# Optimization experiments

Hardware: AMD Instinct MI355X
Metric: run time of the kernel (lower is better)

## Reference

```python
import jax, jax.numpy as jnp
import numpy as np

B, F, N, D, P = 32, 32, 36, 2048, 512  # batch, frames, objects, input dim, projected dim


def setup_inputs() -> dict:
    key = jax.random.key(0)
    ks = jax.random.split(key, 8)
    s = 1.0 / np.sqrt(D).astype(np.float32)  # torch nn.Linear default init range
    u = lambda k, shape: jax.random.uniform(k, shape, jnp.float32, -s, s)
    return {
        "object_variable": jax.random.normal(ks[0], (B, F, N, D), jnp.float32),
        "W_proj": u(ks[1], (D, P)), "b_proj": u(ks[2], (P,)),
        "W_sigma": u(ks[3], (D, P)), "b_sigma": u(ks[4], (P,)),
        "W_psi": u(ks[5], (D, P)), "b_psi": u(ks[6], (P,)),
        "W_r": u(ks[7], (D, P)),  # bias=False
    }


def reference(object_variable, W_proj, b_proj, W_sigma, b_sigma, W_psi, b_psi, W_r):
    # Dropouts are identity in eval mode.
    x = object_variable                                   # [B,F,N,D]
    r_feat = x @ W_proj + b_proj                          # [B,F,N,P]
    sig = x @ W_sigma + b_sigma                           # [B,F,N,P]
    psi = x @ W_psi + b_psi                               # [B,F,N,P]
    a_coeff = jnp.einsum('bfnp,bfmp->bfnm', sig, psi)     # [B,F,N,N] unscaled QK^T
    a_hat = jax.nn.softmax(a_coeff, axis=-1)
    r_hat = jnp.einsum('bfnm,bfmp->bfnp', a_hat, x @ W_r) # AV matmul
    return (r_feat, r_hat)
```

## Files before the change

kernel.cpp:

```cpp
#include <hip/hip_runtime.h>
#include <hip/hip_fp16.h>
#include <stdint.h>

typedef _Float16 half2v __attribute__((ext_vector_type(2)));
typedef _Float16 half4v __attribute__((ext_vector_type(4)));
typedef _Float16 half8v __attribute__((ext_vector_type(8)));
typedef float    float4v __attribute__((ext_vector_type(4)));

#define KDIM 2048
#define PDIM 512
#define MROWS 36864
#define NOBJ 36
#define NTOT 2048

__device__ __forceinline__ void gload_lds16(const void* g, void* l) {
    using gptr_t = const __attribute__((address_space(1))) unsigned int*;
    using lptr_t = __attribute__((address_space(3))) unsigned int*;
    __builtin_amdgcn_global_load_lds((gptr_t)(uintptr_t)g,
                                     (lptr_t)(uint32_t)(uintptr_t)l,
                                     16, 0, 0);
}

__global__ __launch_bounds__(256)
void cvt_x_kernel(const float* __restrict__ x, _Float16* __restrict__ xh) {
    const size_t i = ((size_t)blockIdx.x * 256 + threadIdx.x) * 8;
    float4v a = *(const float4v*)&x[i];
    float4v b = *(const float4v*)&x[i + 4];
    half8v h;
    h[0] = (_Float16)a[0]; h[1] = (_Float16)a[1];
    h[2] = (_Float16)a[2]; h[3] = (_Float16)a[3];
    h[4] = (_Float16)b[0]; h[5] = (_Float16)b[1];
    h[6] = (_Float16)b[2]; h[7] = (_Float16)b[3];
    *(half8v*)&xh[i] = h;
}

__global__ __launch_bounds__(256)
void cvt_w_kernel(const float* __restrict__ Wp, const float* __restrict__ Ws,
                  const float* __restrict__ Wq, const float* __restrict__ Wr,
                  _Float16* __restrict__ wt) {
    const int bid = blockIdx.x;
    const int mat = bid >> 10;
    const int t   = bid & 1023;
    const int kt  = t >> 4;
    const int pt  = t & 15;
    const float* W = (mat == 0) ? Wp : (mat == 1) ? Ws : (mat == 2) ? Wq : Wr;

    __shared__ float tile[32][33];
    const int tx = threadIdx.x & 31;
    const int ty = threadIdx.x >> 5;
    #pragma unroll
    for (int r = 0; r < 4; ++r) {
        const int k = kt * 32 + ty + r * 8;
        tile[ty + r * 8][tx] = W[(size_t)k * PDIM + pt * 32 + tx];
    }
    __syncthreads();
    #pragma unroll
    for (int r = 0; r < 4; ++r) {
        const int p = pt * 32 + ty + r * 8;
        const int n = mat * PDIM + p;
        wt[(size_t)n * KDIM + kt * 32 + tx] = (_Float16)tile[tx][ty + r * 8];
    }
}

__global__ __launch_bounds__(256, 2)
void proj_gemm(const _Float16* __restrict__ A, const _Float16* __restrict__ Bt,
               float* __restrict__ rfeat, _Float16* __restrict__ sg,
               _Float16* __restrict__ ph, _Float16* __restrict__ vh,
               const float* __restrict__ bp, const float* __restrict__ bs,
               const float* __restrict__ bq) {
    __shared__ _Float16 sA[128 * 32];
    __shared__ _Float16 sB[128 * 32];

    const int tid  = threadIdx.x;
    const int lane = tid & 63;
    const int wave = tid >> 6;

    const int n0 = (blockIdx.x & 15) * 128;
    const int m0 = (blockIdx.x >> 4) * 128;

    const int srow = tid >> 2;
    const int skc  = (tid & 3) * 8;
    const _Float16* ga0 = A  + (size_t)(m0 + srow) * KDIM + skc;
    const _Float16* ga1 = A  + (size_t)(m0 + 64 + srow) * KDIM + skc;
    const _Float16* gb0 = Bt + (size_t)(n0 + srow) * KDIM + skc;
    const _Float16* gb1 = Bt + (size_t)(n0 + 64 + srow) * KDIM + skc;

    char* lA = (char*)sA + tid * 16;
    char* lB = (char*)sB + tid * 16;

    const int m_off = (wave >> 1) * 64;
    const int n_off = (wave & 1) * 64;
    const int frow  = lane & 15;
    const int fk    = (lane >> 4) * 8;

    float4v acc[4][4] = {};

    for (int kt = 0; kt < KDIM / 32; ++kt) {
        __syncthreads();
        gload_lds16(ga0, lA);
        gload_lds16(ga1, lA + 4096);
        gload_lds16(gb0, lB);
        gload_lds16(gb1, lB + 4096);
        ga0 += 32; ga1 += 32; gb0 += 32; gb1 += 32;
        __syncthreads();

        half8v af[4], bf[4];
        #pragma unroll
        for (int i = 0; i < 4; ++i)
            af[i] = *(const half8v*)&sA[(m_off + i * 16 + frow) * 32 + fk];
        #pragma unroll
        for (int j = 0; j < 4; ++j)
            bf[j] = *(const half8v*)&sB[(n_off + j * 16 + frow) * 32 + fk];
        #pragma unroll
        for (int i = 0; i < 4; ++i)
            #pragma unroll
            for (int j = 0; j < 4; ++j)
                acc[i][j] = __builtin_amdgcn_mfma_f32_16x16x32_f16(af[i], bf[j], acc[i][j], 0, 0, 0);
    }

    const int seg = n0 >> 9;
    const int pn0 = (n0 & 511) + n_off;
    #pragma unroll
    for (int j = 0; j < 4; ++j) {
        const int pcol = pn0 + j * 16 + frow;
        float bias = 0.0f;
        if (seg == 0)      bias = bp[pcol];
        else if (seg == 1) bias = bs[pcol];
        else if (seg == 2) bias = bq[pcol];
        #pragma unroll
        for (int i = 0; i < 4; ++i) {
            const int rb = m0 + m_off + i * 16 + (lane >> 4) * 4;
            #pragma unroll
            for (int r = 0; r < 4; ++r) {
                const float val = acc[i][j][r] + bias;
                const size_t off = (size_t)(rb + r) * PDIM + pcol;
                if (seg == 0)      rfeat[off] = val;
                else if (seg == 1) sg[off] = (_Float16)val;
                else if (seg == 2) ph[off] = (_Float16)val;
                else               vh[off] = (_Float16)val;
            }
        }
    }
}

__global__ __launch_bounds__(256, 2)
void attn_kernel(const _Float16* __restrict__ sg, const _Float16* __restrict__ ph,
                 const _Float16* __restrict__ vh, float* __restrict__ rhat) {
    __shared__ _Float16 ss[NOBJ * 520];
    __shared__ _Float16 ps[NOBJ * 520];
    __shared__ float    Ls[NOBJ * 37];

    const int tid = threadIdx.x;
    const size_t base = (size_t)blockIdx.x * (NOBJ * PDIM);

    for (int c = tid; c < (NOBJ * PDIM / 8); c += 256) {
        const int row = c >> 6;
        const int col = (c & 63) * 8;
        *(half8v*)&ss[row * 520 + col] = *(const half8v*)&sg[base + row * PDIM + col];
        *(half8v*)&ps[row * 520 + col] = *(const half8v*)&ph[base + row * PDIM + col];
    }
    __syncthreads();

    if (tid < 144) {
        const int i0 = (tid / 12) * 3;
        const int j0 = (tid % 12) * 3;
        float accv[3][3] = {};
        for (int p = 0; p < PDIM; p += 8) {
            half8v si[3], pj[3];
            #pragma unroll
            for (int ii = 0; ii < 3; ++ii) si[ii] = *(const half8v*)&ss[(i0 + ii) * 520 + p];
            #pragma unroll
            for (int jj = 0; jj < 3; ++jj) pj[jj] = *(const half8v*)&ps[(j0 + jj) * 520 + p];
            #pragma unroll
            for (int ii = 0; ii < 3; ++ii)
                #pragma unroll
                for (int jj = 0; jj < 3; ++jj) {
                    float t = accv[ii][jj];
                    #pragma unroll
                    for (int q = 0; q < 4; ++q) {
                        half2v x2; x2[0] = si[ii][2 * q]; x2[1] = si[ii][2 * q + 1];
                        half2v y2; y2[0] = pj[jj][2 * q]; y2[1] = pj[jj][2 * q + 1];
                        t = __builtin_amdgcn_fdot2(x2, y2, t, false);
                    }
                    accv[ii][jj] = t;
                }
        }
        #pragma unroll
        for (int ii = 0; ii < 3; ++ii)
            #pragma unroll
            for (int jj = 0; jj < 3; ++jj)
                Ls[(i0 + ii) * 37 + (j0 + jj)] = accv[ii][jj];
    }
    __syncthreads();

    if (tid < NOBJ) {
        float mx = -1e30f;
        for (int j = 0; j < NOBJ; ++j) mx = fmaxf(mx, Ls[tid * 37 + j]);
        float sum = 0.0f;
        for (int j = 0; j < NOBJ; ++j) {
            float e = __expf(Ls[tid * 37 + j] - mx);
            sum += e;
            Ls[tid * 37 + j] = e;
        }
        const float inv = 1.0f / sum;
        for (int j = 0; j < NOBJ; ++j) Ls[tid * 37 + j] *= inv;
    }
    __syncthreads();

    const int p4 = (tid & 127) * 4;
    const int r0 = tid >> 7;
    float4v acc[18] = {};
    for (int j = 0; j < NOBJ; ++j) {
        half4v v4 = *(const half4v*)&vh[base + (size_t)j * PDIM + p4];
        float4v vf;
        vf[0] = (float)v4[0]; vf[1] = (float)v4[1];
        vf[2] = (float)v4[2]; vf[3] = (float)v4[3];
        #pragma unroll
        for (int m = 0; m < 18; ++m) {
            const float aw = Ls[(2 * m + r0) * 37 + j];
            acc[m] += aw * vf;
        }
    }
    #pragma unroll
    for (int m = 0; m < 18; ++m)
        *(float4v*)&rhat[base + (size_t)(2 * m + r0) * PDIM + p4] = acc[m];
}

extern "C" void kernel_launch(void* const* d_in, const int* in_sizes, int n_in,
                              void* d_out, int out_size, void* d_ws, size_t ws_size,
                              hipStream_t stream) {
    const float* x   = (const float*)d_in[0];
    const float* Wp  = (const float*)d_in[1];
    const float* bp  = (const float*)d_in[2];
    const float* Wsg = (const float*)d_in[3];
    const float* bsg = (const float*)d_in[4];
    const float* Wps = (const float*)d_in[5];
    const float* bps = (const float*)d_in[6];
    const float* Wr  = (const float*)d_in[7];
    float* out = (float*)d_out;

    char* ws = (char*)d_ws;
    _Float16* xh = (_Float16*)(ws);
    _Float16* wt = (_Float16*)(ws + 150994944UL);
    _Float16* sg = (_Float16*)(ws + 159383552UL);
    _Float16* ph = (_Float16*)(ws + 197132288UL);
    _Float16* vh = (_Float16*)(ws + 234881024UL);

    cvt_x_kernel<<<36864, 256, 0, stream>>>(x, xh);
    cvt_w_kernel<<<4096, 256, 0, stream>>>(Wp, Wsg, Wps, Wr, wt);
    proj_gemm<<<288 * 16, 256, 0, stream>>>(xh, wt, out, sg, ph, vh, bp, bsg, bps);
    attn_kernel<<<1024, 256, 0, stream>>>(sg, ph, vh, out + 18874368);
}
```

Baseline: 905.6 us.

## Rewrite projection GEMM with 256x256 tiles, double-buffered LDS and phased MFMA pipeline

The projection GEMM moves from 128x128 tiles with 256 threads and a single LDS buffer to 256x256 tiles with 512 threads, a K step of 64, and double-buffered LDS. Global-to-LDS loads for the next tiles are issued during MFMA phases, with explicit waitcnt, barriers and setprio. The change also adds XOR swizzling of LDS columns to avoid bank conflicts and a block-index swizzle for L2 locality. The aim is to hide memory latency and raise MFMA utilisation, at the cost of more LDS per block (128KB), higher register pressure, and fragile hand-written synchronisation.

```diff
diff --git a/kernel.cpp b/kernel.cpp
--- a/kernel.cpp
+++ b/kernel.cpp
@@ -12,6 +12,7 @@
 #define MROWS 36864
 #define NOBJ 36
 #define NTOT 2048
+#define KT   32
 
 __device__ __forceinline__ void gload_lds16(const void* g, void* l) {
     using gptr_t = const __attribute__((address_space(1))) unsigned int*;
@@ -62,77 +63,150 @@
     }
 }
 
-__global__ __launch_bounds__(256, 2)
+#define BARRIER() __builtin_amdgcn_s_barrier()
+
+#define STAGE_AH(b_, kt_, h_) do {                                            \
+    const _Float16* g_ = pA + (size_t)(kt_) * 64 + (size_t)(h_) * 262144;     \
+    char* l_ = (char*)sA + (b_) * 32768 + (h_) * 16384 + tid * 16;            \
+    gload_lds16(g_, l_);                                                      \
+    gload_lds16(g_ + 131072, l_ + 8192);                                      \
+} while (0)
+
+#define STAGE_BH(b_, kt_, h_) do {                                            \
+    const _Float16* g_ = pB + (size_t)(kt_) * 64 + (size_t)(h_) * 262144;     \
+    char* l_ = (char*)sB + (b_) * 32768 + (h_) * 16384 + tid * 16;            \
+    gload_lds16(g_, l_);                                                      \
+    gload_lds16(g_ + 131072, l_ + 8192);                                      \
+} while (0)
+
+#define LOAD_AF(b_, qm_) do {                                                 \
+    const char* ba_ = (const char*)sA + (b_) * 32768 + wrbase;                \
+    _Pragma("unroll")                                                         \
+    for (int mi = 0; mi < 4; ++mi) {                                          \
+        const int ro_ = ((qm_) * 64 + mi * 16 + r15) * 128;                   \
+        af[mi][0] = *(const half8v*)(ba_ + ro_ + ck0);                        \
+        af[mi][1] = *(const half8v*)(ba_ + ro_ + ck1);                        \
+    }                                                                         \
+} while (0)
+
+#define LOAD_BF(b_, qn_, dst_) do {                                           \
+    const char* bb_ = (const char*)sB + (b_) * 32768 + wcbase;                \
+    _Pragma("unroll")                                                         \
+    for (int ni = 0; ni < 2; ++ni) {                                          \
+        const int ro_ = (rB0 + (qn_) * 32 + ni * 16 + r15) * 128;             \
+        dst_[ni][0] = *(const half8v*)(bb_ + ro_ + ck0);                      \
+        dst_[ni][1] = *(const half8v*)(bb_ + ro_ + ck1);                      \
+    }                                                                         \
+} while (0)
+
+#define MFMA16(mb_, nb_, bf_) do {                                            \
+    _Pragma("unroll")                                                         \
+    for (int mi = 0; mi < 4; ++mi)                                            \
+        _Pragma("unroll")                                                     \
+        for (int ni = 0; ni < 2; ++ni) {                                      \
+            acc[(mb_) + mi][(nb_) + ni] = __builtin_amdgcn_mfma_f32_16x16x32_f16( \
+                af[mi][0], bf_[ni][0], acc[(mb_) + mi][(nb_) + ni], 0, 0, 0); \
+            acc[(mb_) + mi][(nb_) + ni] = __builtin_amdgcn_mfma_f32_16x16x32_f16( \
+                af[mi][1], bf_[ni][1], acc[(mb_) + mi][(nb_) + ni], 0, 0, 0); \
+        }                                                                     \
+} while (0)
+
+#define PHASE_SYNC() do {                                                     \
+    BARRIER();                                                                \
+    asm volatile("s_waitcnt lgkmcnt(0)" ::: "memory");                        \
+    __builtin_amdgcn_sched_barrier(0);                                        \
+} while (0)
+
+#define ITER(t_, b_) do {                                                     \
+                                                        \
+    LOAD_AF(b_, 0); LOAD_BF(b_, 0, b0);                                       \
+    if ((t_) + 1 < KT) STAGE_AH((b_) ^ 1, (t_) + 1, 0);                       \
+    PHASE_SYNC();                                                             \
+    __builtin_amdgcn_s_setprio(1); MFMA16(0, 0, b0);                          \
+    __builtin_amdgcn_s_setprio(0); BARRIER();                                 \
+                                                        \
+    LOAD_BF(b_, 1, b1);                                                       \
+    if ((t_) + 1 < KT) STAGE_AH((b_) ^ 1, (t_) + 1, 1);                       \
+    PHASE_SYNC();                                                             \
+    __builtin_amdgcn_s_setprio(1); MFMA16(0, 2, b1);                          \
+    __builtin_amdgcn_s_setprio(0); BARRIER();                                 \
+                                                        \
+    LOAD_AF(b_, 1);                                                           \
+    if ((t_) + 2 < KT) STAGE_BH(b_, (t_) + 2, 0);                             \
+    PHASE_SYNC();                                                             \
+    __builtin_amdgcn_s_setprio(1); MFMA16(4, 2, b1);                          \
+    __builtin_amdgcn_s_setprio(0); BARRIER();                                 \
+                      \
+    if ((t_) + 2 < KT) STAGE_BH(b_, (t_) + 2, 1);                             \
+    __builtin_amdgcn_s_setprio(1); MFMA16(4, 0, b0);                          \
+    __builtin_amdgcn_s_setprio(0);                                            \
+    if ((t_) + 2 < KT)      { asm volatile("s_waitcnt vmcnt(4)" ::: "memory"); } \
+    else if ((t_) + 1 < KT) { asm volatile("s_waitcnt vmcnt(0)" ::: "memory"); } \
+    BARRIER();                                                                \
+} while (0)
+
+__global__ __launch_bounds__(512, 2)
 void proj_gemm(const _Float16* __restrict__ A, const _Float16* __restrict__ Bt,
                float* __restrict__ rfeat, _Float16* __restrict__ sg,
                _Float16* __restrict__ ph, _Float16* __restrict__ vh,
                const float* __restrict__ bp, const float* __restrict__ bs,
                const float* __restrict__ bq) {
-    __shared__ _Float16 sA[128 * 32];
-    __shared__ _Float16 sB[128 * 32];
+    __shared__ _Float16 sA[2][2][8192];
+    __shared__ _Float16 sB[2][2][8192];
 
     const int tid  = threadIdx.x;
     const int lane = tid & 63;
-    const int wave = tid >> 6;
-
-    const int n0 = (blockIdx.x & 15) * 128;
-    const int m0 = (blockIdx.x >> 4) * 128;
-
-    const int srow = tid >> 2;
-    const int skc  = (tid & 3) * 8;
-    const _Float16* ga0 = A  + (size_t)(m0 + srow) * KDIM + skc;
-    const _Float16* ga1 = A  + (size_t)(m0 + 64 + srow) * KDIM + skc;
-    const _Float16* gb0 = Bt + (size_t)(n0 + srow) * KDIM + skc;
-    const _Float16* gb1 = Bt + (size_t)(n0 + 64 + srow) * KDIM + skc;
-
-    char* lA = (char*)sA + tid * 16;
-    char* lB = (char*)sB + tid * 16;
-
-    const int m_off = (wave >> 1) * 64;
-    const int n_off = (wave & 1) * 64;
-    const int frow  = lane & 15;
-    const int fk    = (lane >> 4) * 8;
-
-    float4v acc[4][4] = {};
-
-    for (int kt = 0; kt < KDIM / 32; ++kt) {
-        __syncthreads();
-        gload_lds16(ga0, lA);
-        gload_lds16(ga1, lA + 4096);
-        gload_lds16(gb0, lB);
-        gload_lds16(gb1, lB + 4096);
-        ga0 += 32; ga1 += 32; gb0 += 32; gb1 += 32;
-        __syncthreads();
-
-        half8v af[4], bf[4];
-        #pragma unroll
-        for (int i = 0; i < 4; ++i)
-            af[i] = *(const half8v*)&sA[(m_off + i * 16 + frow) * 32 + fk];
-        #pragma unroll
-        for (int j = 0; j < 4; ++j)
-            bf[j] = *(const half8v*)&sB[(n_off + j * 16 + frow) * 32 + fk];
-        #pragma unroll
-        for (int i = 0; i < 4; ++i)
-            #pragma unroll
-            for (int j = 0; j < 4; ++j)
-                acc[i][j] = __builtin_amdgcn_mfma_f32_16x16x32_f16(af[i], bf[j], acc[i][j], 0, 0, 0);
+    const int wid  = tid >> 6;
+    const int wr   = wid >> 2;
+    const int wc   = wid & 3;
+    const int r15  = lane & 15;
+    const int k4   = lane >> 4;
+
+    const int bid = blockIdx.x;
+    const int swz = (bid & 7) * 144 + (bid >> 3);
+    const int mt  = swz >> 3, nt = swz & 7;
+    const int m0  = mt * 256, n0 = nt * 256;
+
+    const int srow = tid >> 3;
+    const int sk   = (tid & 7) ^ (srow & 7);
+    const _Float16* pA = A  + (size_t)(m0 + srow) * KDIM + sk * 8;
+    const _Float16* pB = Bt + (size_t)(n0 + srow) * KDIM + sk * 8;
+
+    const int ck0 = ((k4)     ^ (r15 & 7)) * 16;
+    const int ck1 = ((4 + k4) ^ (r15 & 7)) * 16;
+    const int wrbase = wr * 16384;
+    const int wcbase = (wc >> 1) * 16384;
+    const int rB0    = (wc & 1) * 64;
+
+    half8v af[4][2], b0[2][2], b1[2][2];
+    float4v acc[8][4] = {};
+
+    STAGE_AH(0, 0, 0); STAGE_AH(0, 0, 1);
+    STAGE_BH(0, 0, 0); STAGE_BH(0, 0, 1);
+    STAGE_BH(1, 1, 0); STAGE_BH(1, 1, 1);
+    asm volatile("s_waitcnt vmcnt(4)" ::: "memory");
+    BARRIER();
+
+    for (int tt = 0; tt < KT; tt += 2) {
+        ITER(tt, 0);
+        ITER(tt + 1, 1);
     }
 
     const int seg = n0 >> 9;
-    const int pn0 = (n0 & 511) + n_off;
+    const int pn0 = (n0 & 511) + wc * 64;
     #pragma unroll
-    for (int j = 0; j < 4; ++j) {
-        const int pcol = pn0 + j * 16 + frow;
+    for (int ni = 0; ni < 4; ++ni) {
+        const int pcol = pn0 + ni * 16 + r15;
         float bias = 0.0f;
         if (seg == 0)      bias = bp[pcol];
         else if (seg == 1) bias = bs[pcol];
         else if (seg == 2) bias = bq[pcol];
         #pragma unroll
-        for (int i = 0; i < 4; ++i) {
-            const int rb = m0 + m_off + i * 16 + (lane >> 4) * 4;
+        for (int mi = 0; mi < 8; ++mi) {
+            const int rb = m0 + wr * 128 + mi * 16 + k4 * 4;
             #pragma unroll
             for (int r = 0; r < 4; ++r) {
-                const float val = acc[i][j][r] + bias;
+                const float val = acc[mi][ni][r] + bias;
                 const size_t off = (size_t)(rb + r) * PDIM + pcol;
                 if (seg == 0)      rfeat[off] = val;
                 else if (seg == 1) sg[off] = (_Float16)val;
@@ -248,6 +322,6 @@
 
     cvt_x_kernel<<<36864, 256, 0, stream>>>(x, xh);
     cvt_w_kernel<<<4096, 256, 0, stream>>>(Wp, Wsg, Wps, Wr, wt);
-    proj_gemm<<<288 * 16, 256, 0, stream>>>(xh, wt, out, sg, ph, vh, bp, bsg, bps);
+    proj_gemm<<<144 * 8, 512, 0, stream>>>(xh, wt, out, sg, ph, vh, bp, bsg, bps);
     attn_kernel<<<1024, 256, 0, stream>>>(sg, ph, vh, out + 18874368);
 }
```

Result: faster. 851.9 us (-5.9%).
